# Kernel optimization log

Hardware: AMD Instinct MI355X
Metric: run time of the kernel (lower is better)

## Reference

```python
import jax, jax.numpy as jnp
import numpy as np
import math

N_EMBD = 1024
N_HEAD = 16
D_FF = 4 * N_EMBD
B, T = 4, 2048

def gelu_tanh(x):
    return 0.5 * x * (1.0 + jnp.tanh(jnp.sqrt(2.0 / jnp.pi).astype(x.dtype) * (x + 0.044715 * x ** 3)))

def layernorm(x, g, b, eps=1e-5):
    mu = jnp.mean(x, axis=-1, keepdims=True)
    var = jnp.var(x, axis=-1, keepdims=True)
    return (x - mu) * jax.lax.rsqrt(var + eps) * g + b

def setup_inputs() -> dict:
    key = jax.random.key(0)
    ks = jax.random.split(key, 12)
    s = lambda fan_in: 1.0 / np.sqrt(fan_in)
    return {
        "x": jax.random.normal(ks[0], (B, T, N_EMBD), jnp.float32),
        "ln1_g": jnp.ones((N_EMBD,), jnp.float32),
        "ln1_b": jnp.zeros((N_EMBD,), jnp.float32),
        "w_attn": jax.random.normal(ks[1], (N_EMBD, 3 * N_EMBD), jnp.float32) * s(N_EMBD),
        "b_attn": jnp.zeros((3 * N_EMBD,), jnp.float32),
        "w_proj": jax.random.normal(ks[2], (N_EMBD, N_EMBD), jnp.float32) * s(N_EMBD),
        "b_proj": jnp.zeros((N_EMBD,), jnp.float32),
        "ln2_g": jnp.ones((N_EMBD,), jnp.float32),
        "ln2_b": jnp.zeros((N_EMBD,), jnp.float32),
        "w_fc": jax.random.normal(ks[3], (N_EMBD, D_FF), jnp.float32) * s(N_EMBD),
        "b_fc": jnp.zeros((D_FF,), jnp.float32),
        "w_fc2": jax.random.normal(ks[4], (D_FF, N_EMBD), jnp.float32) * s(D_FF),
        "b_fc2": jnp.zeros((N_EMBD,), jnp.float32),
    }

def reference(x, ln1_g, ln1_b, w_attn, b_attn, w_proj, b_proj,
              ln2_g, ln2_b, w_fc, b_fc, w_fc2, b_fc2):
    Bn, Tn, C = x.shape
    hs = C // N_HEAD
    # --- attention ---
    h = layernorm(x, ln1_g, ln1_b)
    qkv = h @ w_attn + b_attn  # [B,T,3C]
    q, k, v = jnp.split(qkv, 3, axis=-1)
    q = q.reshape(Bn, Tn, N_HEAD, hs).transpose(0, 2, 1, 3)
    k = k.reshape(Bn, Tn, N_HEAD, hs).transpose(0, 2, 1, 3)
    v = v.reshape(Bn, Tn, N_HEAD, hs).transpose(0, 2, 1, 3)
    att = jnp.einsum('bhqd,bhkd->bhqk', q, k) * (hs ** -0.5)
    mask = jnp.tril(jnp.ones((Tn, Tn), bool))
    att = jnp.where(mask, att, -jnp.inf)
    att = jax.nn.softmax(att, axis=-1)
    y = jnp.einsum('bhqk,bhkd->bhqd', att, v)
    y = y.transpose(0, 2, 1, 3).reshape(Bn, Tn, C)
    x = x + (y @ w_proj + b_proj)
    # --- MLP ---
    h2 = layernorm(x, ln2_g, ln2_b)
    h2 = gelu_tanh(h2 @ w_fc + b_fc)
    x = x + (h2 @ w_fc2 + b_fc2)
    return x
```

## Files before the change

kernel.cpp:

```cpp
#include <hip/hip_runtime.h>
#include <hip/hip_bf16.h>

#define B_ 4
#define T_ 2048
#define C_ 1024
#define NH_ 16
#define FF_ 4096
#define NT_ (B_*T_)

typedef short bf16x8 __attribute__((ext_vector_type(8)));
typedef float f32x4 __attribute__((ext_vector_type(4)));

#define LDS_AS(p) ((__attribute__((address_space(3))) uint32_t*)(p))
#define GLB_AS(p) ((const __attribute__((address_space(1))) uint32_t*)(p))

__device__ __forceinline__ float bf2f(__hip_bfloat16 v){ return __bfloat162float(v); }
__device__ __forceinline__ __hip_bfloat16 f2bf(float f){ return __float2bfloat16(f); }

__device__ __forceinline__ f32x4 mfma16(bf16x8 a, bf16x8 b, f32x4 c){
  return __builtin_amdgcn_mfma_f32_16x16x32_bf16(a, b, c, 0, 0, 0);
}

__global__ __launch_bounds__(256) void transpose_bf16(const float* __restrict__ in,
                                                      __hip_bfloat16* __restrict__ out,
                                                      int K, int N) {
  __shared__ float tile[32][33];
  const int n0 = blockIdx.x * 32, k0 = blockIdx.y * 32;
  const int x = threadIdx.x & 31, y = threadIdx.x >> 5;
  #pragma unroll
  for (int i = 0; i < 4; i++)
    tile[y + 8*i][x] = in[(size_t)(k0 + y + 8*i) * N + n0 + x];
  __syncthreads();
  #pragma unroll
  for (int i = 0; i < 4; i++)
    out[(size_t)(n0 + y + 8*i) * K + k0 + x] = f2bf(tile[x][y + 8*i]);
}

__global__ __launch_bounds__(256) void ln_bf16(const float* __restrict__ x,
                                               const float* __restrict__ g,
                                               const float* __restrict__ b,
                                               __hip_bfloat16* __restrict__ out) {
  const int row = blockIdx.x;
  const int tid = threadIdx.x;
  float4 v = ((const float4*)(x + (size_t)row * C_))[tid];
  float s  = v.x + v.y + v.z + v.w;
  float s2 = v.x*v.x + v.y*v.y + v.z*v.z + v.w*v.w;
  #pragma unroll
  for (int off = 32; off > 0; off >>= 1) {
    s  += __shfl_down(s,  off, 64);
    s2 += __shfl_down(s2, off, 64);
  }
  __shared__ float red[8];
  const int w = tid >> 6, l = tid & 63;
  if (l == 0) { red[w] = s; red[4 + w] = s2; }
  __syncthreads();
  s  = red[0] + red[1] + red[2] + red[3];
  s2 = red[4] + red[5] + red[6] + red[7];
  const float mu   = s * (1.0f / C_);
  const float var  = s2 * (1.0f / C_) - mu * mu;
  const float rstd = rsqrtf(var + 1e-5f);
  float4 gv = ((const float4*)g)[tid];
  float4 bv = ((const float4*)b)[tid];
  ushort4 o;
  __hip_bfloat16 t;
  t = f2bf((v.x - mu) * rstd * gv.x + bv.x); o.x = *(unsigned short*)&t;
  t = f2bf((v.y - mu) * rstd * gv.y + bv.y); o.y = *(unsigned short*)&t;
  t = f2bf((v.z - mu) * rstd * gv.z + bv.z); o.z = *(unsigned short*)&t;
  t = f2bf((v.w - mu) * rstd * gv.w + bv.w); o.w = *(unsigned short*)&t;
  ((ushort4*)out)[(size_t)row * (C_/4) + tid] = o;
}

template <int MODE, int BM>
__global__ __launch_bounds__(512, 2) void gemm256(const __hip_bfloat16* __restrict__ A,
                                                  const __hip_bfloat16* __restrict__ BT,
                                                  const float* __restrict__ bias,
                                                  const float* __restrict__ resid,
                                                  void* __restrict__ outp,
                                                  void* __restrict__ outp2,
                                                  int N, int K) {
  constexpr int MF = BM / 32;
  constexpr int AJ = (BM == 256) ? 4 : 2;
  __shared__ __hip_bfloat16 Als[2][BM * 64];
  __shared__ __hip_bfloat16 Bls[2][256 * 64];
  const int tid = threadIdx.x;
  const int w = tid >> 6, l = tid & 63;
  const int wm = w >> 2, wn = w & 3;
  const int m_ = l & 15, q_ = l >> 4;
  const int lrow8 = l >> 3;
  const int gchunk = (l & 7) ^ lrow8;

  const int nwg = gridDim.x;
  const int bid = blockIdx.x;
  const int swz = (bid & 7) * (nwg >> 3) + (bid >> 3);
  const int nbx = N >> 8;
  const int tile_n = (swz % nbx) * 256;
  const int tile_m = (swz / nbx) * BM;

  const int arow0 = (BM == 256) ? (wm * 128 + wn * 32) : (wm * 64 + wn * 16);
  const int brow0 = (wn >> 1) * 128 + (wm * 2 + (wn & 1)) * 32;

  f32x4 acc[MF][4] = {};

#define STAGE256(buf_, k0_) do {                                                   \
    _Pragma("unroll")                                                              \
    for (int j = 0; j < AJ; j++) {                                                 \
      const int rg = arow0 + j*8;                                                  \
      __builtin_amdgcn_global_load_lds(                                            \
        GLB_AS(A + (size_t)(tile_m + rg + lrow8) * K + (k0_) + gchunk*8),          \
        LDS_AS(&Als[buf_][rg*64]), 16, 0, 0);                                      \
    }                                                                              \
    _Pragma("unroll")                                                              \
    for (int j = 0; j < 4; j++) {                                                  \
      const int rg = brow0 + j*8;                                                  \
      __builtin_amdgcn_global_load_lds(                                            \
        GLB_AS(BT + (size_t)(tile_n + rg + lrow8) * K + (k0_) + gchunk*8),         \
        LDS_AS(&Bls[buf_][rg*64]), 16, 0, 0);                                      \
    }                                                                              \
  } while (0)

  STAGE256(0, 0);
  __syncthreads();

  const int nt = K >> 6;
  int cur = 0;
  #pragma unroll 1
  for (int t = 0; t < nt; t++) {
    if (t + 1 < nt) STAGE256(cur ^ 1, (t + 1) * 64);

    bf16x8 bfr[2][4];
    #pragma unroll
    for (int kc = 0; kc < 2; kc++)
      #pragma unroll
      for (int ni = 0; ni < 4; ni++) {
        const int row = wn*64 + ni*16 + m_;
        bfr[kc][ni] = *(const bf16x8*)&Bls[cur][row*64 + (((kc*4 + q_) ^ (row & 7)) * 8)];
      }
    #pragma unroll
    for (int mi = 0; mi < MF; mi++) {
      const int row = wm*(BM/2) + mi*16 + m_;
      const bf16x8 a0 = *(const bf16x8*)&Als[cur][row*64 + ((q_       ^ (row & 7)) * 8)];
      const bf16x8 a1 = *(const bf16x8*)&Als[cur][row*64 + (((4 + q_) ^ (row & 7)) * 8)];
      #pragma unroll
      for (int ni = 0; ni < 4; ni++) acc[mi][ni] = mfma16(a0, bfr[0][ni], acc[mi][ni]);
      #pragma unroll
      for (int ni = 0; ni < 4; ni++) acc[mi][ni] = mfma16(a1, bfr[1][ni], acc[mi][ni]);
    }
    __syncthreads();
    cur ^= 1;
  }
#undef STAGE256

  const int r0 = tile_m + wm * (BM/2) + q_ * 4;
  const int c0 = tile_n + wn * 64 + m_;
  #pragma unroll
  for (int mi = 0; mi < MF; mi++) {
    #pragma unroll
    for (int r = 0; r < 4; r++) {
      const int row = r0 + mi * 16 + r;
      #pragma unroll
      for (int ni = 0; ni < 4; ni++) {
        const int col = c0 + ni * 16;
        float v = acc[mi][ni][r] + bias[col];
        if (MODE == 0) {
          if (tile_n < 2 * C_) {
            ((__hip_bfloat16*)outp)[(size_t)row * (2*C_) + col] = f2bf(v);
          } else {
            const int dg = col - 2 * C_;
            ((__hip_bfloat16*)outp2)[((size_t)((row >> 11) * 1024 + dg)) * T_ + (row & 2047)] = f2bf(v);
          }
        } else if (MODE == 1 || MODE == 3) {
          ((float*)outp)[(size_t)row * N + col] = resid[(size_t)row * N + col] + v;
        } else {
          const float u = 0.7978845608028654f * (v + 0.044715f * v * v * v);
          const float e = __expf(2.0f * u);
          ((__hip_bfloat16*)outp)[(size_t)row * N + col] = f2bf(v * (1.0f - 1.0f / (e + 1.0f)));
        }
      }
    }
  }
}

__global__ __launch_bounds__(256, 4) void flash_attn(const __hip_bfloat16* __restrict__ qk,
                                                     const __hip_bfloat16* __restrict__ vT,
                                                     __hip_bfloat16* __restrict__ y) {
  const int id  = blockIdx.x;
  const int xcd = id & 7;
  const int jj  = id >> 3;
  const int bh  = xcd * 8 + (jj >> 4);
  const int p   = jj & 15;
  const int b   = bh >> 4, h = bh & 15;
  const int tid = threadIdx.x, w = tid >> 6, l = tid & 63;
  const int m_ = l & 15, q_ = l >> 4;
  const int lrow8 = l >> 3;
  const int gchunk = (l & 7) ^ lrow8;

  __shared__ __hip_bfloat16 Kls[2][64 * 64];
  __shared__ __hip_bfloat16 Vls[64 * 64];
  __shared__ __hip_bfloat16 Pls[64 * 76];

  const size_t kgbase = (size_t)b * T_ * (2*C_) + C_ + h*64;
  const size_t vgbase = (size_t)bh * 64 * T_;

#define STAGE_K(kt_, buf_) do {                                                        \
    _Pragma("unroll")                                                                  \
    for (int j2 = 0; j2 < 2; j2++) {                                                   \
      const int rg = j2*32 + w*8;                                                      \
      __builtin_amdgcn_global_load_lds(                                                \
        GLB_AS(qk + kgbase + (size_t)((kt_)*64 + rg + lrow8)*(2*C_) + gchunk*8),       \
        LDS_AS(&Kls[buf_][rg*64]), 16, 0, 0);                                          \
    }                                                                                  \
  } while (0)

#define STAGE_V(kt_) do {                                                              \
    _Pragma("unroll")                                                                  \
    for (int j2 = 0; j2 < 2; j2++) {                                                   \
      const int rg = j2*32 + w*8;                                                      \
      __builtin_amdgcn_global_load_lds(                                                \
        GLB_AS(vT + vgbase + (size_t)(rg + lrow8)*T_ + (kt_)*64 + gchunk*8),           \
        LDS_AS(&Vls[rg*64]), 16, 0, 0);                                                \
    }                                                                                  \
  } while (0)

  #pragma unroll 1
  for (int ui = 0; ui < 2; ui++) {
    const int qt = ui ? (31 - p) : p;
    const int q0 = qt * 64;

    bf16x8 aq[2];
    {
      const float qscale = 0.125f * 1.44269504088896f;
      const size_t qbase = ((size_t)b * T_ + q0 + w*16 + m_) * (2*C_) + h*64;
      #pragma unroll
      for (int kh = 0; kh < 2; kh++) {
        union { uint4 u; __hip_bfloat16 h8[8]; } t;
        t.u = *(const uint4*)&qk[qbase + kh*32 + q_*8];
        __hip_bfloat16 a[8];
        #pragma unroll
        for (int jx = 0; jx < 8; jx++) a[jx] = f2bf(bf2f(t.h8[jx]) * qscale);
        aq[kh] = *(const bf16x8*)a;
      }
    }

    f32x4 accO[4] = {};
    float lsum[4] = {0.f, 0.f, 0.f, 0.f};

    STAGE_K(0, 0);
    asm volatile("s_waitcnt vmcnt(0)" ::: "memory");
    __builtin_amdgcn_s_barrier();

    int cur = 0;
    #pragma unroll 1
    for (int kt = 0; kt <= qt; kt++) {
      STAGE_V(kt);

      f32x4 s[4];
      #pragma unroll
      for (int ni = 0; ni < 4; ni++) {
        const int row = ni*16 + m_;
        const bf16x8 bk0 = *(const bf16x8*)&Kls[cur][row*64 + ((q_     ^ (row & 7)) * 8)];
        const bf16x8 bk1 = *(const bf16x8*)&Kls[cur][row*64 + (((4+q_) ^ (row & 7)) * 8)];
        f32x4 z = {};
        z = mfma16(aq[0], bk0, z);
        s[ni] = mfma16(aq[1], bk1, z);
      }

      if (kt < qt) STAGE_K(kt + 1, cur ^ 1);

      if (kt == qt) {
        const int qrow = w*16 + q_*4;
        #pragma unroll
        for (int ni = 0; ni < 4; ni++) {
          const int kcol = ni*16 + m_;
          #pragma unroll
          for (int r = 0; r < 4; r++)
            if (kcol > qrow + r) s[ni][r] = -1e30f;
        }
      }

      #pragma unroll
      for (int ni = 0; ni < 4; ni++)
        #pragma unroll
        for (int r = 0; r < 4; r++)
          s[ni][r] = exp2f(s[ni][r]);
      #pragma unroll
      for (int r = 0; r < 4; r++)
        lsum[r] += (s[0][r] + s[1][r]) + (s[2][r] + s[3][r]);
      #pragma unroll
      for (int ni = 0; ni < 4; ni++)
        #pragma unroll
        for (int r = 0; r < 4; r++)
          Pls[(w*16 + q_*4 + r) * 76 + ni*16 + m_] = f2bf(s[ni][r]);

      bf16x8 ap[2];
      ap[0] = *(const bf16x8*)&Pls[(w*16 + m_) * 76 + q_*8];
      ap[1] = *(const bf16x8*)&Pls[(w*16 + m_) * 76 + 32 + q_*8];

      if (kt < qt) asm volatile("s_waitcnt vmcnt(2)" ::: "memory");
      else         asm volatile("s_waitcnt vmcnt(0)" ::: "memory");
      __builtin_amdgcn_s_barrier();

      #pragma unroll
      for (int ni = 0; ni < 4; ni++) {
        const int row = ni*16 + m_;
        const bf16x8 bv0 = *(const bf16x8*)&Vls[row*64 + ((q_     ^ (row & 7)) * 8)];
        const bf16x8 bv1 = *(const bf16x8*)&Vls[row*64 + (((4+q_) ^ (row & 7)) * 8)];
        accO[ni] = mfma16(ap[0], bv0, accO[ni]);
        accO[ni] = mfma16(ap[1], bv1, accO[ni]);
      }

      asm volatile("s_waitcnt vmcnt(0) lgkmcnt(0)" ::: "memory");
      __builtin_amdgcn_s_barrier();
      cur ^= 1;
    }

    #pragma unroll
    for (int r = 0; r < 4; r++) {
      #pragma unroll
      for (int d = 1; d < 16; d <<= 1)
        lsum[r] += __shfl_xor(lsum[r], d, 64);
    }

    const size_t ybase = ((size_t)b * T_ + q0) * C_ + h*64;
    #pragma unroll
    for (int r = 0; r < 4; r++) {
      const int row = w*16 + q_*4 + r;
      const float linv = 1.0f / lsum[r];
      #pragma unroll
      for (int ni = 0; ni < 4; ni++)
        y[ybase + (size_t)row * C_ + ni*16 + m_] = f2bf(accO[ni][r] * linv);
    }
  }
#undef STAGE_K
#undef STAGE_V
}

extern "C" void kernel_launch(void* const* d_in, const int* in_sizes, int n_in,
                              void* d_out, int out_size, void* d_ws, size_t ws_size,
                              hipStream_t stream) {
  const float* x      = (const float*)d_in[0];
  const float* ln1_g  = (const float*)d_in[1];
  const float* ln1_b  = (const float*)d_in[2];
  const float* w_attn = (const float*)d_in[3];
  const float* b_attn = (const float*)d_in[4];
  const float* w_proj = (const float*)d_in[5];
  const float* b_proj = (const float*)d_in[6];
  const float* ln2_g  = (const float*)d_in[7];
  const float* ln2_b  = (const float*)d_in[8];
  const float* w_fc   = (const float*)d_in[9];
  const float* b_fc   = (const float*)d_in[10];
  const float* w_fc2  = (const float*)d_in[11];
  const float* b_fc2  = (const float*)d_in[12];
  float* out = (float*)d_out;

  char* ws = (char*)d_ws;
  const size_t MB = 1024 * 1024;
  __hip_bfloat16* h      = (__hip_bfloat16*)(ws);
  __hip_bfloat16* qk     = (__hip_bfloat16*)(ws + 16*MB);
  __hip_bfloat16* vT     = (__hip_bfloat16*)(ws + 48*MB);
  __hip_bfloat16* y      = (__hip_bfloat16*)(ws + 64*MB);
  float*          x2     = (float*)        (ws + 80*MB);
  __hip_bfloat16* h2     = (__hip_bfloat16*)(ws + 64*MB);
  __hip_bfloat16* gbuf   = (__hip_bfloat16*)(ws);
  __hip_bfloat16* wattnT = (__hip_bfloat16*)(ws + 112*MB);
  __hip_bfloat16* wprojT = (__hip_bfloat16*)(ws + 118*MB);
  __hip_bfloat16* wfcT   = (__hip_bfloat16*)(ws + 120*MB);
  __hip_bfloat16* wfc2T  = (__hip_bfloat16*)(ws + 128*MB);

  transpose_bf16<<<dim3(3*C_/32, C_/32), 256, 0, stream>>>(w_attn, wattnT, C_, 3*C_);
  transpose_bf16<<<dim3(C_/32,  C_/32), 256, 0, stream>>>(w_proj, wprojT, C_, C_);
  transpose_bf16<<<dim3(FF_/32, C_/32), 256, 0, stream>>>(w_fc,   wfcT,   C_, FF_);
  transpose_bf16<<<dim3(C_/32, FF_/32), 256, 0, stream>>>(w_fc2,  wfc2T,  FF_, C_);

  ln_bf16<<<NT_, 256, 0, stream>>>(x, ln1_g, ln1_b, h);
  gemm256<0,128><<<dim3(768), 512, 0, stream>>>(h, wattnT, b_attn, nullptr, qk, vT, 3*C_, C_);
  flash_attn<<<dim3(1024), 256, 0, stream>>>(qk, vT, y);
  gemm256<1,128><<<dim3(256), 512, 0, stream>>>(y, wprojT, b_proj, x, x2, nullptr, C_, C_);
  ln_bf16<<<NT_, 256, 0, stream>>>(x2, ln2_g, ln2_b, h2);
  gemm256<2,256><<<dim3(512), 512, 0, stream>>>(h2, wfcT, b_fc, nullptr, gbuf, nullptr, FF_, C_);
  gemm256<3,128><<<dim3(256), 512, 0, stream>>>(gbuf, wfc2T, b_fc2, x2, out, nullptr, C_, FF_);
}
```

Baseline: 526.2 us.

## Triple-buffer GEMM LDS pipeline with vmcnt waits and XCD-aware tile mapping

Reworks the shared GEMM kernel into a 3-stage LDS pipeline that prefetches two k-tiles ahead, using explicit vmcnt waits and raw barriers in place of __syncthreads. It also fixes BM at 128 (so the FC GEMM launches 1024 blocks), raises MFMA priority with setprio, and adds a per-XCD grouped tile mapping (CW) to improve L2 reuse. Three buffers of 48KB each cut occupancy to one block per CU (launch bounds 512,1), trading latency hiding through occupancy for deeper prefetch.

```diff
diff --git a/kernel.cpp b/kernel.cpp
--- a/kernel.cpp
+++ b/kernel.cpp
@@ -70,18 +70,16 @@
   ((ushort4*)out)[(size_t)row * (C_/4) + tid] = o;
 }
 
-template <int MODE, int BM>
-__global__ __launch_bounds__(512, 2) void gemm256(const __hip_bfloat16* __restrict__ A,
+template <int MODE>
+__global__ __launch_bounds__(512, 1) void gemm256(const __hip_bfloat16* __restrict__ A,
                                                   const __hip_bfloat16* __restrict__ BT,
                                                   const float* __restrict__ bias,
                                                   const float* __restrict__ resid,
                                                   void* __restrict__ outp,
                                                   void* __restrict__ outp2,
-                                                  int N, int K) {
-  constexpr int MF = BM / 32;
-  constexpr int AJ = (BM == 256) ? 4 : 2;
-  __shared__ __hip_bfloat16 Als[2][BM * 64];
-  __shared__ __hip_bfloat16 Bls[2][256 * 64];
+                                                  int N, int K, int CW) {
+  __shared__ __hip_bfloat16 Als[3][128 * 64];
+  __shared__ __hip_bfloat16 Bls[3][256 * 64];
   const int tid = threadIdx.x;
   const int w = tid >> 6, l = tid & 63;
   const int wm = w >> 2, wn = w & 3;
@@ -89,43 +87,50 @@
   const int lrow8 = l >> 3;
   const int gchunk = (l & 7) ^ lrow8;
 
-  const int nwg = gridDim.x;
+  const int nbx = N >> 8;
   const int bid = blockIdx.x;
-  const int swz = (bid & 7) * (nwg >> 3) + (bid >> 3);
-  const int nbx = N >> 8;
-  const int tile_n = (swz % nbx) * 256;
-  const int tile_m = (swz / nbx) * BM;
-
-  const int arow0 = (BM == 256) ? (wm * 128 + wn * 32) : (wm * 64 + wn * 16);
-  const int brow0 = (wn >> 1) * 128 + (wm * 2 + (wn & 1)) * 32;
-
-  f32x4 acc[MF][4] = {};
-
-#define STAGE256(buf_, k0_) do {                                                   \
+  const int x8 = bid & 7, i8 = bid >> 3;
+  const int ccols = nbx / CW;
+  const int RH = (int)(gridDim.x >> 3) / CW;
+  const int tile_n = ((x8 % ccols) * CW + (i8 % CW)) << 8;
+  const int tile_m = ((x8 / ccols) * RH + (i8 / CW)) << 7;
+
+  f32x4 acc[4][4] = {};
+
+#define STAGE3(buf_, k0_) do {                                                     \
     _Pragma("unroll")                                                              \
-    for (int j = 0; j < AJ; j++) {                                                 \
-      const int rg = arow0 + j*8;                                                  \
+    for (int j = 0; j < 2; j++) {                                                  \
+      const int rg = w*16 + j*8;                                                   \
       __builtin_amdgcn_global_load_lds(                                            \
         GLB_AS(A + (size_t)(tile_m + rg + lrow8) * K + (k0_) + gchunk*8),          \
         LDS_AS(&Als[buf_][rg*64]), 16, 0, 0);                                      \
     }                                                                              \
     _Pragma("unroll")                                                              \
     for (int j = 0; j < 4; j++) {                                                  \
-      const int rg = brow0 + j*8;                                                  \
+      const int rg = w*32 + j*8;                                                   \
       __builtin_amdgcn_global_load_lds(                                            \
         GLB_AS(BT + (size_t)(tile_n + rg + lrow8) * K + (k0_) + gchunk*8),         \
         LDS_AS(&Bls[buf_][rg*64]), 16, 0, 0);                                      \
     }                                                                              \
   } while (0)
 
-  STAGE256(0, 0);
-  __syncthreads();
-
   const int nt = K >> 6;
+  STAGE3(0, 0);
+  STAGE3(1, 64);
+
   int cur = 0;
   #pragma unroll 1
   for (int t = 0; t < nt; t++) {
-    if (t + 1 < nt) STAGE256(cur ^ 1, (t + 1) * 64);
+    const int nxt2 = (cur + 2 >= 3) ? cur - 1 : cur + 2;
+    if (t + 2 < nt) {
+      STAGE3(nxt2, (t + 2) * 64);
+      asm volatile("s_waitcnt vmcnt(12)" ::: "memory");
+    } else if (t + 1 < nt) {
+      asm volatile("s_waitcnt vmcnt(6)" ::: "memory");
+    } else {
+      asm volatile("s_waitcnt vmcnt(0)" ::: "memory");
+    }
+    __builtin_amdgcn_s_barrier();
 
     bf16x8 bfr[2][4];
     #pragma unroll
@@ -135,9 +140,10 @@
         const int row = wn*64 + ni*16 + m_;
         bfr[kc][ni] = *(const bf16x8*)&Bls[cur][row*64 + (((kc*4 + q_) ^ (row & 7)) * 8)];
       }
-    #pragma unroll
-    for (int mi = 0; mi < MF; mi++) {
-      const int row = wm*(BM/2) + mi*16 + m_;
+    __builtin_amdgcn_s_setprio(1);
+    #pragma unroll
+    for (int mi = 0; mi < 4; mi++) {
+      const int row = wm*64 + mi*16 + m_;
       const bf16x8 a0 = *(const bf16x8*)&Als[cur][row*64 + ((q_       ^ (row & 7)) * 8)];
       const bf16x8 a1 = *(const bf16x8*)&Als[cur][row*64 + (((4 + q_) ^ (row & 7)) * 8)];
       #pragma unroll
@@ -145,15 +151,16 @@
       #pragma unroll
       for (int ni = 0; ni < 4; ni++) acc[mi][ni] = mfma16(a1, bfr[1][ni], acc[mi][ni]);
     }
-    __syncthreads();
-    cur ^= 1;
+    __builtin_amdgcn_s_setprio(0);
+    __builtin_amdgcn_s_barrier();
+    cur = (cur + 1 >= 3) ? 0 : cur + 1;
   }
-#undef STAGE256
-
-  const int r0 = tile_m + wm * (BM/2) + q_ * 4;
+#undef STAGE3
+
+  const int r0 = tile_m + wm * 64 + q_ * 4;
   const int c0 = tile_n + wn * 64 + m_;
   #pragma unroll
-  for (int mi = 0; mi < MF; mi++) {
+  for (int mi = 0; mi < 4; mi++) {
     #pragma unroll
     for (int r = 0; r < 4; r++) {
       const int row = r0 + mi * 16 + r;
@@ -372,10 +379,10 @@
   transpose_bf16<<<dim3(C_/32, FF_/32), 256, 0, stream>>>(w_fc2,  wfc2T,  FF_, C_);
 
   ln_bf16<<<NT_, 256, 0, stream>>>(x, ln1_g, ln1_b, h);
-  gemm256<0,128><<<dim3(768), 512, 0, stream>>>(h, wattnT, b_attn, nullptr, qk, vT, 3*C_, C_);
+  gemm256<0><<<dim3(768), 512, 0, stream>>>(h, wattnT, b_attn, nullptr, qk, vT, 3*C_, C_, 6);
   flash_attn<<<dim3(1024), 256, 0, stream>>>(qk, vT, y);
-  gemm256<1,128><<<dim3(256), 512, 0, stream>>>(y, wprojT, b_proj, x, x2, nullptr, C_, C_);
+  gemm256<1><<<dim3(256), 512, 0, stream>>>(y, wprojT, b_proj, x, x2, nullptr, C_, C_, 4);
   ln_bf16<<<NT_, 256, 0, stream>>>(x2, ln2_g, ln2_b, h2);
-  gemm256<2,256><<<dim3(512), 512, 0, stream>>>(h2, wfcT, b_fc, nullptr, gbuf, nullptr, FF_, C_);
-  gemm256<3,128><<<dim3(256), 512, 0, stream>>>(gbuf, wfc2T, b_fc2, x2, out, nullptr, C_, FF_);
-}
+  gemm256<2><<<dim3(1024), 512, 0, stream>>>(h2, wfcT, b_fc, nullptr, gbuf, nullptr, FF_, C_, 4);
+  gemm256<3><<<dim3(256), 512, 0, stream>>>(gbuf, wfc2T, b_fc2, x2, out, nullptr, C_, FF_, 4);
+}
```

New measurement: 554.6 us. +5.4%, slower.
